# Optimization experiments

Measured on AMD Instinct MI355X. Metric: run time of the kernel, lower is better.

The kernel has to match this reference:

```python
import jax, jax.numpy as jnp
import numpy as np
import math

B, Z, D = 1024, 32768, 128

def setup_inputs() -> dict:
    key = jax.random.key(0)
    k1, k2, k3 = jax.random.split(key, 3)
    z_sparse = jax.random.randint(k1, (B, Z), 0, 2, dtype=jnp.int32)
    context_embedding = jax.random.normal(k2, (B, D), dtype=jnp.float32)
    embd_table = jax.random.normal(k3, (Z, D), dtype=jnp.float32)  # nn.Embedding weight
    return {"z_sparse": z_sparse, "context_embedding": context_embedding, "embd_table": embd_table}

def reference(z_sparse, context_embedding, embd_table):
    # mask[b, z] = feature z active in batch b  (matches (z_sparse > 0).nonzero())
    mask = z_sparse > 0  # [B, Z]
    # attn_scores = (ctx * emb).sum(-1) / sqrt(D), densified over all (b, z)
    scores = (context_embedding @ embd_table.T) / math.sqrt(embd_table.shape[1])  # [B, Z]
    # per-batch softmax over active features only
    masked = jnp.where(mask, scores, -jnp.inf)
    w = jax.nn.softmax(masked, axis=-1)
    w = jnp.where(mask, w, 0.0)  # zero inactive (also kills NaN for all-empty rows)
    # scatter-add of emb * weight == weighted matmul against the table
    out = w @ embd_table  # [B, D]
    counts = jnp.clip(jnp.sum(mask, axis=-1), 1, None)  # bincount(...).clamp(min=1)
    return out / counts[:, None].astype(out.dtype)
```

## Files before the change

kernel.cpp:

```cpp
#include <hip/hip_runtime.h>
#include <stdint.h>

#define B_SZ 1024
#define Z_SZ 32768
#define D_SZ 128
#define NZ   64
#define CZ   (Z_SZ / NZ)
#define TZ   64
#define ITERS (CZ / TZ)
#define TBLK 128
#define NWAVE 4
#define WROWS 32

#define SEMB_STRIDE  136
#define SEMBT_STRIDE 72
#define SP_STRIDE    72
#define ST_STRIDE    136

#define NB_TAB  (Z_SZ / 64)

#define WS_O   0
#define WS_M   (NZ * B_SZ * D_SZ)
#define WS_L   (WS_M + NZ * B_SZ)
#define WS_C   (WS_L + NZ * B_SZ)
#define WS_TAB (WS_C + NZ * B_SZ)

typedef short bf16x8  __attribute__((ext_vector_type(8)));
typedef float f32x4   __attribute__((ext_vector_type(4)));
typedef float f32x16  __attribute__((ext_vector_type(16)));

#if __has_builtin(__builtin_amdgcn_exp2f)
#define EXP2F(x) __builtin_amdgcn_exp2f(x)
#else
#define EXP2F(x) exp2f(x)
#endif

__device__ __forceinline__ unsigned short f2bf(float f) {
    union { float f; uint32_t u; } v; v.f = f;
    uint32_t u = v.u;
    u = (u + 0x7FFFu + ((u >> 16) & 1u)) >> 16;
    return (unsigned short)u;
}

__global__ __launch_bounds__(256) void prep(
    const float*    __restrict__ emb,
    unsigned short* __restrict__ embR,
    unsigned short* __restrict__ embT)
{
    __shared__ __align__(16) unsigned short st[64 * ST_STRIDE];
    const int z0 = blockIdx.x * 64;
    const int t  = threadIdx.x;
    {
        const int r = t >> 2, q = t & 3;
        const float* src = emb + (size_t)(z0 + r) * D_SZ + q * 32;
        unsigned short* dR = embR + (size_t)(z0 + r) * D_SZ + q * 32;
        unsigned short* dL = st + r * ST_STRIDE + q * 32;
#pragma unroll
        for (int u = 0; u < 8; ++u) {
            float4 x = *(const float4*)(src + 4 * u);
            ushort4 h;
            h.x = f2bf(x.x); h.y = f2bf(x.y); h.z = f2bf(x.z); h.w = f2bf(x.w);
            *(ushort4*)(dR + 4 * u) = h;
            *(ushort4*)(dL + 4 * u) = h;
        }
    }
    __syncthreads();
    {
        const int lane = t & 63, w = t >> 6;
#pragma unroll
        for (int i = 0; i < 4; ++i) {
            const int d = w * 32 + i * 8 + (lane >> 3);
            const int c = lane & 7;
            bf16x8 v;
#pragma unroll
            for (int k = 0; k < 8; ++k) v[k] = (short)st[(c * 8 + k) * ST_STRIDE + d];
            *(bf16x8*)(embT + (size_t)d * Z_SZ + z0 + c * 8) = v;
        }
    }
}

__global__ __launch_bounds__(256, 2) void attn_part(
    const int*            __restrict__ zs,
    const float*          __restrict__ ctx,
    const unsigned short* __restrict__ embR,
    const unsigned short* __restrict__ embT,
    float*                __restrict__ ws)
{
    __shared__ __align__(16) unsigned short s_emb [TZ   * SEMB_STRIDE];
    __shared__ __align__(16) unsigned short s_embT[D_SZ * SEMBT_STRIDE];
    __shared__ __align__(16) unsigned short s_P   [NWAVE * WROWS * SP_STRIDE];

    const int tid  = threadIdx.x;
    const int wave = tid >> 6;
    const int lane = tid & 63;
    const int l31  = lane & 31;
    const int hi   = lane >> 5;

    const int bg     = blockIdx.x;
    const int ch     = blockIdx.y;
    const int z_base = ch * CZ;
    const int wb0    = bg * TBLK + wave * WROWS;
    const int brow   = wb0 + l31;

    const int srow = tid >> 2, sq3 = tid & 3;
    const int sd   = tid >> 1, sh  = tid & 1;

    const int* zrow = zs + (size_t)brow * Z_SZ + hi * 4;

    bf16x8 afrag[8];
    {
        const float scale = (float)(1.4426950408889634 * 0.08838834764831845);
        const float* crow = ctx + (size_t)brow * D_SZ;
#pragma unroll
        for (int ks = 0; ks < 8; ++ks) {
            const float* p = crow + ks * 16 + hi * 8;
            float4 x0 = *(const float4*)(p);
            float4 x1 = *(const float4*)(p + 4);
            bf16x8 a;
            a[0] = (short)f2bf(x0.x * scale); a[1] = (short)f2bf(x0.y * scale);
            a[2] = (short)f2bf(x0.z * scale); a[3] = (short)f2bf(x0.w * scale);
            a[4] = (short)f2bf(x1.x * scale); a[5] = (short)f2bf(x1.y * scale);
            a[6] = (short)f2bf(x1.z * scale); a[7] = (short)f2bf(x1.w * scale);
            afrag[ks] = a;
        }
    }

    float m_s = -1e30f, l_s = 0.f;
    int   cnt = 0;
    f32x16 acc[4];
#pragma unroll
    for (int n = 0; n < 4; ++n) {
#pragma unroll
        for (int e = 0; e < 16; ++e) acc[n][e] = 0.f;
    }

    int4 mc[2][4], mn[2][4];
#pragma unroll
    for (int nt = 0; nt < 2; ++nt)
#pragma unroll
        for (int g = 0; g < 4; ++g)
            mc[nt][g] = *(const int4*)(zrow + z_base + nt * 32 + g * 8);

    for (int it = 0; it < ITERS; ++it) {
        const int z0 = z_base + it * TZ;
        __syncthreads();

        {
            const unsigned short* srcR = embR + (size_t)(z0 + srow) * D_SZ + sq3 * 32;
            unsigned short* dst = s_emb + srow * SEMB_STRIDE + sq3 * 32;
            bf16x8 v0 = *(const bf16x8*)(srcR);      bf16x8 v1 = *(const bf16x8*)(srcR + 8);
            bf16x8 v2 = *(const bf16x8*)(srcR + 16); bf16x8 v3 = *(const bf16x8*)(srcR + 24);
            *(bf16x8*)(dst)      = v0; *(bf16x8*)(dst + 8)  = v1;
            *(bf16x8*)(dst + 16) = v2; *(bf16x8*)(dst + 24) = v3;
        }
        {
            const unsigned short* srcT = embT + (size_t)sd * Z_SZ + z0 + sh * 32;
            unsigned short* dst = s_embT + sd * SEMBT_STRIDE + sh * 32;
            bf16x8 v0 = *(const bf16x8*)(srcT);      bf16x8 v1 = *(const bf16x8*)(srcT + 8);
            bf16x8 v2 = *(const bf16x8*)(srcT + 16); bf16x8 v3 = *(const bf16x8*)(srcT + 24);
            *(bf16x8*)(dst)      = v0; *(bf16x8*)(dst + 8)  = v1;
            *(bf16x8*)(dst + 16) = v2; *(bf16x8*)(dst + 24) = v3;
        }

        __syncthreads();

        if (it + 1 < ITERS) {
            const int z0n = z0 + TZ;
#pragma unroll
            for (int nt = 0; nt < 2; ++nt)
#pragma unroll
                for (int g = 0; g < 4; ++g)
                    mn[nt][g] = *(const int4*)(zrow + z0n + nt * 32 + g * 8);
        }

        f32x16 sfr[2];
#pragma unroll
        for (int nt = 0; nt < 2; ++nt) {
            f32x16 c;
#pragma unroll
            for (int e = 0; e < 16; ++e) c[e] = 0.f;
            const unsigned short* bb = s_emb + (nt * 32 + l31) * SEMB_STRIDE + hi * 8;
#pragma unroll
            for (int ks = 0; ks < 8; ++ks) {
                bf16x8 ef = *(const bf16x8*)(bb + ks * 16);
                c = __builtin_amdgcn_mfma_f32_32x32x16_bf16(ef, afrag[ks], c, 0, 0, 0);
            }
            sfr[nt] = c;
        }

        int bit[2][16];
#pragma unroll
        for (int nt = 0; nt < 2; ++nt) {
#pragma unroll
            for (int g = 0; g < 4; ++g) {
                bit[nt][4*g+0] = (mc[nt][g].x > 0) ? 1 : 0;
                bit[nt][4*g+1] = (mc[nt][g].y > 0) ? 1 : 0;
                bit[nt][4*g+2] = (mc[nt][g].z > 0) ? 1 : 0;
                bit[nt][4*g+3] = (mc[nt][g].w > 0) ? 1 : 0;
                cnt += bit[nt][4*g+0] + bit[nt][4*g+1] + bit[nt][4*g+2] + bit[nt][4*g+3];
            }
        }

        float tm = -1e30f;
#pragma unroll
        for (int nt = 0; nt < 2; ++nt) {
#pragma unroll
            for (int r = 0; r < 16; r += 4) {
                float a0 = bit[nt][r+0] ? sfr[nt][r+0] : -1e30f;
                float a1 = bit[nt][r+1] ? sfr[nt][r+1] : -1e30f;
                float a2 = bit[nt][r+2] ? sfr[nt][r+2] : -1e30f;
                float a3 = bit[nt][r+3] ? sfr[nt][r+3] : -1e30f;
                tm = fmaxf(tm, fmaxf(fmaxf(a0, a1), fmaxf(a2, a3)));
            }
        }
        tm = fmaxf(tm, __shfl_xor(tm, 32));

        if (__any(tm > m_s + 8.f)) {
            float mnew = fmaxf(m_s, tm);
            float al = EXP2F(m_s - mnew);
            m_s = mnew;
            l_s *= al;
#pragma unroll
            for (int n = 0; n < 4; ++n)
#pragma unroll
                for (int e = 0; e < 16; ++e) acc[n][e] *= al;
        }

        unsigned short* pwv = s_P + wave * (WROWS * SP_STRIDE) + l31 * SP_STRIDE + hi * 4;
        float ps = 0.f;
#pragma unroll
        for (int nt = 0; nt < 2; ++nt) {
#pragma unroll
            for (int g = 0; g < 4; ++g) {
                float p0 = bit[nt][4*g+0] ? EXP2F(sfr[nt][4*g+0] - m_s) : 0.f;
                float p1 = bit[nt][4*g+1] ? EXP2F(sfr[nt][4*g+1] - m_s) : 0.f;
                float p2 = bit[nt][4*g+2] ? EXP2F(sfr[nt][4*g+2] - m_s) : 0.f;
                float p3 = bit[nt][4*g+3] ? EXP2F(sfr[nt][4*g+3] - m_s) : 0.f;
                ps += (p0 + p1) + (p2 + p3);
                ushort4 h;
                h.x = f2bf(p0); h.y = f2bf(p1); h.z = f2bf(p2); h.w = f2bf(p3);
                *(ushort4*)(pwv + nt * 32 + g * 8) = h;
            }
        }
        ps += __shfl_xor(ps, 32);
        l_s += ps;

        const unsigned short* pb = s_P + wave * (WROWS * SP_STRIDE) + l31 * SP_STRIDE + hi * 8;
        bf16x8 pfrag[4];
#pragma unroll
        for (int ks2 = 0; ks2 < 4; ++ks2) pfrag[ks2] = *(const bf16x8*)(pb + ks2 * 16);
#pragma unroll
        for (int nt2 = 0; nt2 < 4; ++nt2) {
            const unsigned short* tb = s_embT + (nt2 * 32 + l31) * SEMBT_STRIDE + hi * 8;
#pragma unroll
            for (int ks2 = 0; ks2 < 4; ++ks2) {
                bf16x8 ta = *(const bf16x8*)(tb + ks2 * 16);
                acc[nt2] = __builtin_amdgcn_mfma_f32_32x32x16_bf16(ta, pfrag[ks2], acc[nt2], 0, 0, 0);
            }
        }

#pragma unroll
        for (int nt = 0; nt < 2; ++nt)
#pragma unroll
            for (int g = 0; g < 4; ++g) mc[nt][g] = mn[nt][g];
    }

    {
        float* orow = ws + WS_O + ((size_t)ch * B_SZ + brow) * D_SZ;
#pragma unroll
        for (int nt2 = 0; nt2 < 4; ++nt2) {
#pragma unroll
            for (int g = 0; g < 4; ++g) {
                f32x4 v;
                v[0] = acc[nt2][4*g+0]; v[1] = acc[nt2][4*g+1];
                v[2] = acc[nt2][4*g+2]; v[3] = acc[nt2][4*g+3];
                *(f32x4*)(orow + nt2 * 32 + g * 8 + hi * 4) = v;
            }
        }
    }
    cnt += __shfl_xor(cnt, 32);
    if (lane < 32) {
        ws[WS_M + ch * B_SZ + brow] = m_s;
        ws[WS_L + ch * B_SZ + brow] = l_s;
        ws[WS_C + ch * B_SZ + brow] = (float)cnt;
    }
}

__global__ __launch_bounds__(128) void attn_reduce(
    const float* __restrict__ ws, float* __restrict__ out)
{
    const int b = blockIdx.x;
    const int d = threadIdx.x;
    const float* mP = ws + WS_M;
    const float* lP = ws + WS_L;
    const float* cP = ws + WS_C;

    float M = -1e30f;
#pragma unroll
    for (int c = 0; c < NZ; ++c) M = fmaxf(M, mP[c * B_SZ + b]);

    float L = 0.f, C = 0.f, acc = 0.f;
#pragma unroll
    for (int c = 0; c < NZ; ++c) {
        float w = EXP2F(mP[c * B_SZ + b] - M);
        L += lP[c * B_SZ + b] * w;
        C += cP[c * B_SZ + b];
        acc += ws[WS_O + ((size_t)c * B_SZ + b) * D_SZ + d] * w;
    }
    float cntv = fmaxf(C, 1.0f);
    out[(size_t)b * D_SZ + d] = (L > 0.f) ? acc / (L * cntv) : 0.f;
}

extern "C" void kernel_launch(void* const* d_in, const int* in_sizes, int n_in,
                              void* d_out, int out_size, void* d_ws, size_t ws_size,
                              hipStream_t stream) {
    (void)in_sizes; (void)n_in; (void)out_size; (void)ws_size;
    const int*   zs  = (const int*)  d_in[0];
    const float* ctx = (const float*)d_in[1];
    const float* emb = (const float*)d_in[2];
    float* out = (float*)d_out;
    float* ws  = (float*)d_ws;

    unsigned short* embR = (unsigned short*)(ws + WS_TAB);
    unsigned short* embT = embR + (size_t)Z_SZ * D_SZ;

    prep<<<NB_TAB, 256, 0, stream>>>(emb, embR, embT);

    dim3 grid1(B_SZ / TBLK, NZ);
    attn_part<<<grid1, 256, 0, stream>>>(zs, ctx, embR, embT, ws);
    attn_reduce<<<B_SZ, 128, 0, stream>>>(ws, out);
}
```

Before: 239.7 us.

## Double-buffer embedding tiles in LDS and build P fragments via lane shuffles

Splits the shared embedding tiles into two buffers and prefetches the next tile's global data into registers, writing it to the alternate buffer after the MFMA work. This removes one barrier per iteration and hides global load latency behind compute. The probability fragment for the second matmul is now assembled with cross-half-wave shuffles instead of a round trip through shared memory. In exchange it uses more registers for prefetch, and LDS use roughly doubles for the embedding tiles (minus the removed P buffer), which may limit occupancy at two blocks per CU.

```diff
diff --git a/kernel.cpp b/kernel.cpp
--- a/kernel.cpp
+++ b/kernel.cpp
@@ -14,7 +14,6 @@
 
 #define SEMB_STRIDE  136
 #define SEMBT_STRIDE 72
-#define SP_STRIDE    72
 #define ST_STRIDE    136
 
 #define NB_TAB  (Z_SZ / 64)
@@ -40,6 +39,9 @@
     uint32_t u = v.u;
     u = (u + 0x7FFFu + ((u >> 16) & 1u)) >> 16;
     return (unsigned short)u;
+}
+__device__ __forceinline__ uint32_t packbf(float a, float b) {
+    return (uint32_t)f2bf(a) | ((uint32_t)f2bf(b) << 16);
 }
 
 __global__ __launch_bounds__(256) void prep(
@@ -86,12 +88,10 @@
     const unsigned short* __restrict__ embT,
     float*                __restrict__ ws)
 {
-    __shared__ __align__(16) unsigned short s_emb [TZ   * SEMB_STRIDE];
-    __shared__ __align__(16) unsigned short s_embT[D_SZ * SEMBT_STRIDE];
-    __shared__ __align__(16) unsigned short s_P   [NWAVE * WROWS * SP_STRIDE];
+    __shared__ __align__(16) unsigned short s_embA [2][TZ   * SEMB_STRIDE];
+    __shared__ __align__(16) unsigned short s_embTA[2][D_SZ * SEMBT_STRIDE];
 
     const int tid  = threadIdx.x;
-    const int wave = tid >> 6;
     const int lane = tid & 63;
     const int l31  = lane & 31;
     const int hi   = lane >> 5;
@@ -99,7 +99,7 @@
     const int bg     = blockIdx.x;
     const int ch     = blockIdx.y;
     const int z_base = ch * CZ;
-    const int wb0    = bg * TBLK + wave * WROWS;
+    const int wb0    = bg * TBLK + (tid >> 6) * WROWS;
     const int brow   = wb0 + l31;
 
     const int srow = tid >> 2, sq3 = tid & 3;
@@ -129,43 +129,50 @@
     int   cnt = 0;
     f32x16 acc[4];
 #pragma unroll
-    for (int n = 0; n < 4; ++n) {
+    for (int n = 0; n < 4; ++n)
 #pragma unroll
         for (int e = 0; e < 16; ++e) acc[n][e] = 0.f;
-    }
-
-    int4 mc[2][4], mn[2][4];
-#pragma unroll
-    for (int nt = 0; nt < 2; ++nt)
-#pragma unroll
-        for (int g = 0; g < 4; ++g)
-            mc[nt][g] = *(const int4*)(zrow + z_base + nt * 32 + g * 8);
-
+
+    bf16x8 rA[4], rT[4];
+    int4   mc[2][4], mn[2][4];
+
+    {
+        const unsigned short* srcR = embR + (size_t)(z_base + srow) * D_SZ + sq3 * 32;
+        const unsigned short* srcT = embT + (size_t)sd * Z_SZ + z_base + sh * 32;
+#pragma unroll
+        for (int u = 0; u < 4; ++u) { rA[u] = *(const bf16x8*)(srcR + u * 8); }
+#pragma unroll
+        for (int u = 0; u < 4; ++u) { rT[u] = *(const bf16x8*)(srcT + u * 8); }
+#pragma unroll
+        for (int nt = 0; nt < 2; ++nt)
+#pragma unroll
+            for (int g = 0; g < 4; ++g)
+                mc[nt][g] = *(const int4*)(zrow + z_base + nt * 32 + g * 8);
+    }
+    {
+        unsigned short* dA = s_embA[0] + srow * SEMB_STRIDE + sq3 * 32;
+        unsigned short* dT = s_embTA[0] + sd * SEMBT_STRIDE + sh * 32;
+#pragma unroll
+        for (int u = 0; u < 4; ++u) *(bf16x8*)(dA + u * 8) = rA[u];
+#pragma unroll
+        for (int u = 0; u < 4; ++u) *(bf16x8*)(dT + u * 8) = rT[u];
+    }
+    if (ITERS > 1) {
+        const int z1 = z_base + TZ;
+        const unsigned short* srcR = embR + (size_t)(z1 + srow) * D_SZ + sq3 * 32;
+        const unsigned short* srcT = embT + (size_t)sd * Z_SZ + z1 + sh * 32;
+#pragma unroll
+        for (int u = 0; u < 4; ++u) { rA[u] = *(const bf16x8*)(srcR + u * 8); }
+#pragma unroll
+        for (int u = 0; u < 4; ++u) { rT[u] = *(const bf16x8*)(srcT + u * 8); }
+    }
+
+    int cur = 0;
     for (int it = 0; it < ITERS; ++it) {
-        const int z0 = z_base + it * TZ;
         __syncthreads();
 
-        {
-            const unsigned short* srcR = embR + (size_t)(z0 + srow) * D_SZ + sq3 * 32;
-            unsigned short* dst = s_emb + srow * SEMB_STRIDE + sq3 * 32;
-            bf16x8 v0 = *(const bf16x8*)(srcR);      bf16x8 v1 = *(const bf16x8*)(srcR + 8);
-            bf16x8 v2 = *(const bf16x8*)(srcR + 16); bf16x8 v3 = *(const bf16x8*)(srcR + 24);
-            *(bf16x8*)(dst)      = v0; *(bf16x8*)(dst + 8)  = v1;
-            *(bf16x8*)(dst + 16) = v2; *(bf16x8*)(dst + 24) = v3;
-        }
-        {
-            const unsigned short* srcT = embT + (size_t)sd * Z_SZ + z0 + sh * 32;
-            unsigned short* dst = s_embT + sd * SEMBT_STRIDE + sh * 32;
-            bf16x8 v0 = *(const bf16x8*)(srcT);      bf16x8 v1 = *(const bf16x8*)(srcT + 8);
-            bf16x8 v2 = *(const bf16x8*)(srcT + 16); bf16x8 v3 = *(const bf16x8*)(srcT + 24);
-            *(bf16x8*)(dst)      = v0; *(bf16x8*)(dst + 8)  = v1;
-            *(bf16x8*)(dst + 16) = v2; *(bf16x8*)(dst + 24) = v3;
-        }
-
-        __syncthreads();
-
         if (it + 1 < ITERS) {
-            const int z0n = z0 + TZ;
+            const int z0n = z_base + (it + 1) * TZ;
 #pragma unroll
             for (int nt = 0; nt < 2; ++nt)
 #pragma unroll
@@ -173,13 +180,16 @@
                     mn[nt][g] = *(const int4*)(zrow + z0n + nt * 32 + g * 8);
         }
 
+        const unsigned short* se = s_embA[cur];
+        const unsigned short* st_ = s_embTA[cur];
+
         f32x16 sfr[2];
 #pragma unroll
         for (int nt = 0; nt < 2; ++nt) {
             f32x16 c;
 #pragma unroll
             for (int e = 0; e < 16; ++e) c[e] = 0.f;
-            const unsigned short* bb = s_emb + (nt * 32 + l31) * SEMB_STRIDE + hi * 8;
+            const unsigned short* bb = se + (nt * 32 + l31) * SEMB_STRIDE + hi * 8;
 #pragma unroll
             for (int ks = 0; ks < 8; ++ks) {
                 bf16x8 ef = *(const bf16x8*)(bb + ks * 16);
@@ -226,7 +236,7 @@
                 for (int e = 0; e < 16; ++e) acc[n][e] *= al;
         }
 
-        unsigned short* pwv = s_P + wave * (WROWS * SP_STRIDE) + l31 * SP_STRIDE + hi * 4;
+        uint32_t q[8][2];
         float ps = 0.f;
 #pragma unroll
         for (int nt = 0; nt < 2; ++nt) {
@@ -237,21 +247,31 @@
                 float p2 = bit[nt][4*g+2] ? EXP2F(sfr[nt][4*g+2] - m_s) : 0.f;
                 float p3 = bit[nt][4*g+3] ? EXP2F(sfr[nt][4*g+3] - m_s) : 0.f;
                 ps += (p0 + p1) + (p2 + p3);
-                ushort4 h;
-                h.x = f2bf(p0); h.y = f2bf(p1); h.z = f2bf(p2); h.w = f2bf(p3);
-                *(ushort4*)(pwv + nt * 32 + g * 8) = h;
+                q[4*nt+g][0] = packbf(p0, p1);
+                q[4*nt+g][1] = packbf(p2, p3);
             }
         }
         ps += __shfl_xor(ps, 32);
         l_s += ps;
 
-        const unsigned short* pb = s_P + wave * (WROWS * SP_STRIDE) + l31 * SP_STRIDE + hi * 8;
         bf16x8 pfrag[4];
 #pragma unroll
-        for (int ks2 = 0; ks2 < 4; ++ks2) pfrag[ks2] = *(const bf16x8*)(pb + ks2 * 16);
+        for (int ks2 = 0; ks2 < 4; ++ks2) {
+            uint32_t s0 = hi ? q[2*ks2][0] : q[2*ks2+1][0];
+            uint32_t s1 = hi ? q[2*ks2][1] : q[2*ks2+1][1];
+            uint32_t r0 = (uint32_t)__shfl_xor((int)s0, 32);
+            uint32_t r1 = (uint32_t)__shfl_xor((int)s1, 32);
+            union { uint32_t u[4]; bf16x8 v; } P;
+            P.u[0] = hi ? r0 : q[2*ks2][0];
+            P.u[1] = hi ? r1 : q[2*ks2][1];
+            P.u[2] = hi ? q[2*ks2+1][0] : r0;
+            P.u[3] = hi ? q[2*ks2+1][1] : r1;
+            pfrag[ks2] = P.v;
+        }
+
 #pragma unroll
         for (int nt2 = 0; nt2 < 4; ++nt2) {
-            const unsigned short* tb = s_embT + (nt2 * 32 + l31) * SEMBT_STRIDE + hi * 8;
+            const unsigned short* tb = st_ + (nt2 * 32 + l31) * SEMBT_STRIDE + hi * 8;
 #pragma unroll
             for (int ks2 = 0; ks2 < 4; ++ks2) {
                 bf16x8 ta = *(const bf16x8*)(tb + ks2 * 16);
@@ -259,10 +279,29 @@
             }
         }
 
+        if (it + 1 < ITERS) {
+            unsigned short* dA = s_embA[cur ^ 1] + srow * SEMB_STRIDE + sq3 * 32;
+            unsigned short* dT = s_embTA[cur ^ 1] + sd * SEMBT_STRIDE + sh * 32;
+#pragma unroll
+            for (int u = 0; u < 4; ++u) *(bf16x8*)(dA + u * 8) = rA[u];
+#pragma unroll
+            for (int u = 0; u < 4; ++u) *(bf16x8*)(dT + u * 8) = rT[u];
+            if (it + 2 < ITERS) {
+                const int z2 = z_base + (it + 2) * TZ;
+                const unsigned short* srcR = embR + (size_t)(z2 + srow) * D_SZ + sq3 * 32;
+                const unsigned short* srcT = embT + (size_t)sd * Z_SZ + z2 + sh * 32;
+#pragma unroll
+                for (int u = 0; u < 4; ++u) { rA[u] = *(const bf16x8*)(srcR + u * 8); }
+#pragma unroll
+                for (int u = 0; u < 4; ++u) { rT[u] = *(const bf16x8*)(srcT + u * 8); }
+            }
+        }
+
 #pragma unroll
         for (int nt = 0; nt < 2; ++nt)
 #pragma unroll
             for (int g = 0; g < 4; ++g) mc[nt][g] = mn[nt][g];
+        cur ^= 1;
     }
 
     {
```

Measured after the change: 236.8 us. Within noise of the previous version (-1.2%).
